# Performance work log

Measured on AMD Instinct MI355X. Metric: run time of the kernel, lower is better.

Reference implementation:

```python
import jax, jax.numpy as jnp
import numpy as np

B, S, D, H = 2, 2048, 512, 8
DK = D // H
DECAY = 0.02
LN_EPS = 1e-5


def setup_inputs() -> dict:
    key = jax.random.key(0)
    ks = jax.random.split(key, 16)
    sd = 1.0 / np.sqrt(D)
    def lin(k, fan_in, fan_out):
        return jax.random.uniform(k, (fan_in, fan_out), jnp.float32, -sd, sd)
    return {
        "x": jax.random.normal(ks[0], (B, S, D), jnp.float32),
        "wq": lin(ks[1], D, D), "bq": jnp.zeros((D,), jnp.float32),
        "wk": lin(ks[2], D, D), "bk": jnp.zeros((D,), jnp.float32),
        "wv": lin(ks[3], D, D), "bv": jnp.zeros((D,), jnp.float32),
        "wo": lin(ks[4], D, D), "bo": jnp.zeros((D,), jnp.float32),
        "g1_w": lin(ks[5], D, D // 2), "g1_b": jnp.zeros((D // 2,), jnp.float32),
        "g2_w": lin(ks[6], D // 2, 1), "g2_b": jnp.zeros((1,), jnp.float32),
        "ln_g": jnp.ones((D,), jnp.float32), "ln_b": jnp.zeros((D,), jnp.float32),
    }


def _temporal_bias(seq_len):
    # exp(-decay * |i-j|) masked to lower triangle (causal), additive bias
    pos = jnp.arange(seq_len)
    dist = jnp.abs(pos[:, None] - pos[None, :]).astype(jnp.float32)
    bias = jnp.exp(-DECAY * dist)
    return jnp.tril(bias)  # (S, S)


def reference(x, wq, bq, wk, bk, wv, bv, wo, bo, g1_w, g1_b, g2_w, g2_b, ln_g, ln_b):
    b, s, d = x.shape
    # projections -> (B, H, S, DK)
    q = (x @ wq + bq).reshape(b, s, H, DK).transpose(0, 2, 1, 3)
    k = (x @ wk + bk).reshape(b, s, H, DK).transpose(0, 2, 1, 3)
    v = (x @ wv + bv).reshape(b, s, H, DK).transpose(0, 2, 1, 3)
    scores = jnp.einsum("bhqd,bhkd->bhqk", q, k) / jnp.sqrt(jnp.float32(DK))
    scores = scores + _temporal_bias(s)[None, None, :, :]
    attn = jax.nn.softmax(scores, axis=-1)  # (B, H, S, S)
    out = jnp.einsum("bhqk,bhkd->bhqd", attn, v)
    out = out.transpose(0, 2, 1, 3).reshape(b, s, d)
    out = out @ wo + bo
    # gated residual
    gate = jax.nn.sigmoid(jax.nn.relu(x @ g1_w + g1_b) @ g2_w + g2_b)  # (B, S, 1)
    out = out * gate + x * (1.0 - gate)
    # layer norm
    mu = jnp.mean(out, axis=-1, keepdims=True)
    var = jnp.var(out, axis=-1, keepdims=True)
    y = (out - mu) / jnp.sqrt(var + LN_EPS) * ln_g + ln_b
    return (y, attn)
```

## Files before the change

kernel.cpp:

```cpp
#include <hip/hip_runtime.h>

#define BB 2
#define SS 2048
#define DD 512
#define HH 8
#define DKK 64
#define NROWS (BB * SS)
#define Y_SIZE (BB * SS * DD)

typedef __attribute__((ext_vector_type(8))) short short8;
typedef __attribute__((ext_vector_type(4))) float f32x4;

__device__ __forceinline__ ushort f2bf(float f) {
  union { float f; unsigned u; } v; v.f = f;
  unsigned u = v.u;
  return (ushort)((u + 0x7fffu + ((u >> 16) & 1u)) >> 16);
}

__device__ __forceinline__ float bf2f(ushort u) {
  union { unsigned u; float f; } v; v.u = ((unsigned)u) << 16;
  return v.f;
}


__global__ __launch_bounds__(256) void conv_x_kernel(const float* __restrict__ x,
                                                     ushort* __restrict__ xb) {
  int i = (blockIdx.x * 256 + threadIdx.x) * 4;
  float4 v = *(const float4*)(x + i);
  ushort4 o = {f2bf(v.x), f2bf(v.y), f2bf(v.z), f2bf(v.w)};
  *(ushort4*)(xb + i) = o;
}

__global__ __launch_bounds__(256) void conv_wt_kernel(
    const float* __restrict__ w0, const float* __restrict__ w1,
    const float* __restrict__ w2, const float* __restrict__ w3,
    ushort* __restrict__ o0, ushort* __restrict__ o1,
    ushort* __restrict__ o2, ushort* __restrict__ o3) {
  __shared__ float T[64][65];
  const float* w; ushort* wt;
  switch (blockIdx.z) {
    case 0: w = w0; wt = o0; break;
    case 1: w = w1; wt = o1; break;
    case 2: w = w2; wt = o2; break;
    default: w = w3; wt = o3; break;
  }
  const int t = threadIdx.x;
  const int n0 = blockIdx.x * 64, k0 = blockIdx.y * 64;
#pragma unroll
  for (int i = 0; i < 4; ++i) {
    int c = t + i * 256;
    int row = c >> 4, cc = c & 15;
    float4 v = *(const float4*)(w + (size_t)(k0 + row) * DD + n0 + cc * 4);
    T[row][cc * 4 + 0] = v.x; T[row][cc * 4 + 1] = v.y;
    T[row][cc * 4 + 2] = v.z; T[row][cc * 4 + 3] = v.w;
  }
  __syncthreads();
#pragma unroll
  for (int i = 0; i < 2; ++i) {
    int c = t + i * 256;
    int nr = c >> 3, kc = c & 7;
    ushort4 a, b;
    a.x = f2bf(T[kc * 8 + 0][nr]); a.y = f2bf(T[kc * 8 + 1][nr]);
    a.z = f2bf(T[kc * 8 + 2][nr]); a.w = f2bf(T[kc * 8 + 3][nr]);
    b.x = f2bf(T[kc * 8 + 4][nr]); b.y = f2bf(T[kc * 8 + 5][nr]);
    b.z = f2bf(T[kc * 8 + 6][nr]); b.w = f2bf(T[kc * 8 + 7][nr]);
    *(ushort4*)(wt + (size_t)(n0 + nr) * DD + k0 + kc * 8) = a;
    *(ushort4*)(wt + (size_t)(n0 + nr) * DD + k0 + kc * 8 + 4) = b;
  }
}


__device__ __forceinline__ void mfma_gemm64(
    const ushort* __restrict__ A, int lda, const ushort* __restrict__ B, int ldb,
    int K, ushort (*As)[72], ushort (*Bs)[72], f32x4 (&acc)[2][2], int t) {
  const int l = t & 63, w = t >> 6;
  const int mq = w & 1, nq = w >> 1;
  const int l15 = l & 15, l4 = l >> 4;
  for (int k0 = 0; k0 < K; k0 += 64) {
    __syncthreads();
#pragma unroll
    for (int i = 0; i < 2; ++i) {
      int c = t + i * 256;
      int row = c >> 3, cc = c & 7;
      *(uint4*)&As[row][cc * 8] = *(const uint4*)(A + (size_t)row * lda + k0 + cc * 8);
      *(uint4*)&Bs[row][cc * 8] = *(const uint4*)(B + (size_t)row * ldb + k0 + cc * 8);
    }
    __syncthreads();
    short8 af[2][2], bf[2][2];
#pragma unroll
    for (int mt = 0; mt < 2; ++mt)
#pragma unroll
      for (int ks = 0; ks < 2; ++ks)
        af[mt][ks] = *(const short8*)&As[32 * mq + 16 * mt + l15][ks * 32 + l4 * 8];
#pragma unroll
    for (int nt = 0; nt < 2; ++nt)
#pragma unroll
      for (int ks = 0; ks < 2; ++ks)
        bf[nt][ks] = *(const short8*)&Bs[32 * nq + 16 * nt + l15][ks * 32 + l4 * 8];
#pragma unroll
    for (int mt = 0; mt < 2; ++mt)
#pragma unroll
      for (int nt = 0; nt < 2; ++nt)
#pragma unroll
        for (int ks = 0; ks < 2; ++ks)
          acc[mt][nt] = __builtin_amdgcn_mfma_f32_16x16x32_bf16(
              af[mt][ks], bf[nt][ks], acc[mt][nt], 0, 0, 0);
  }
}


__global__ __launch_bounds__(256) void proj_qkv_kernel(
    const ushort* __restrict__ xb,
    const ushort* __restrict__ wqt, const float* __restrict__ bq,
    const ushort* __restrict__ wkt, const float* __restrict__ bk,
    const ushort* __restrict__ wvt, const float* __restrict__ bv,
    ushort* __restrict__ qb, ushort* __restrict__ kb, ushort* __restrict__ vt) {
  __shared__ ushort As[64][72], Bs[64][72];
  const ushort* W; const float* bias; ushort* out;
  if (blockIdx.z == 0) { W = wqt; bias = bq; out = qb; }
  else if (blockIdx.z == 1) { W = wkt; bias = bk; out = kb; }
  else { W = wvt; bias = bv; out = vt; }
  const float scale = (blockIdx.z == 0) ? 0.125f : 1.0f;
  const int m0 = blockIdx.x * 64;
  const int h = blockIdx.y;
  const int t = threadIdx.x;
  const int l = t & 63, w = t >> 6;
  const int mq = w & 1, nq = w >> 1;
  const int l15 = l & 15, l4 = l >> 4;
  f32x4 acc[2][2] = {};
  mfma_gemm64(xb + (size_t)m0 * DD, DD, W + (size_t)h * DKK * DD, DD, DD,
              As, Bs, acc, t);
  float biasv[2];
#pragma unroll
  for (int nt = 0; nt < 2; ++nt) biasv[nt] = bias[h * DKK + 32 * nq + 16 * nt + l15];

  if (blockIdx.z < 2) {
    __syncthreads();
#pragma unroll
    for (int mt = 0; mt < 2; ++mt)
#pragma unroll
      for (int nt = 0; nt < 2; ++nt)
#pragma unroll
        for (int r = 0; r < 4; ++r)
          As[32 * mq + 16 * mt + l4 * 4 + r][32 * nq + 16 * nt + l15] =
              f2bf((acc[mt][nt][r] + biasv[nt]) * scale);
    __syncthreads();
#pragma unroll
    for (int i = 0; i < 2; ++i) {
      int c = t + i * 256;
      int row = c >> 3, cc = c & 7;
      int m = m0 + row, b = m >> 11, s = m & (SS - 1);
      uint4 v = *(const uint4*)&As[row][cc * 8];
      *(uint4*)(out + ((size_t)(b * HH + h) * SS + s) * DKK + cc * 8) = v;
    }
  } else {
#pragma unroll
    for (int mt = 0; mt < 2; ++mt)
#pragma unroll
      for (int nt = 0; nt < 2; ++nt) {
        int dk = 32 * nq + 16 * nt + l15;
        int m = m0 + 32 * mq + 16 * mt + l4 * 4;
        int b = m >> 11, sb = m & (SS - 1);
        ushort4 pk;
        pk.x = f2bf(acc[mt][nt][0] + biasv[nt]);
        pk.y = f2bf(acc[mt][nt][1] + biasv[nt]);
        pk.z = f2bf(acc[mt][nt][2] + biasv[nt]);
        pk.w = f2bf(acc[mt][nt][3] + biasv[nt]);
        *(ushort4*)(out + ((size_t)(b * HH + h) * DKK + dk) * SS + sb) = pk;
      }
  }
}


template <int BF16P>
__global__ __launch_bounds__(256) void attn_kernel(
    const ushort* __restrict__ qb, const ushort* __restrict__ kb,
    const ushort* __restrict__ vt, void* __restrict__ pout,
    float* __restrict__ invb, ushort* __restrict__ ctx) {
  __shared__ ushort Ks[64][72], Vs[64][72], Ps[64][72];
  __shared__ float rs[64];
  const int t = threadIdx.x;
  const int l = t & 63, w = t >> 6;
  const int mq = w & 1, nq = w >> 1;
  const int l15 = l & 15, l4 = l >> 4;
  const int z = blockIdx.x;
  const int q0 = blockIdx.y * 64;
  if (t < 64) rs[t] = 0.f;

  short8 qf[2][2];
#pragma unroll
  for (int bt = 0; bt < 2; ++bt)
#pragma unroll
    for (int ks = 0; ks < 2; ++ks)
      qf[bt][ks] = *(const short8*)(qb +
          ((size_t)z * SS + q0 + 32 * mq + 16 * bt + l15) * DKK + ks * 32 + l4 * 8);

  int qi_[2]; float rowf[2];
#pragma unroll
  for (int bt = 0; bt < 2; ++bt) {
    qi_[bt] = q0 + 32 * mq + 16 * bt + l15;
    rowf[bt] = __expf(-0.02f * (float)qi_[bt]);
  }
  const float c_r[4] = {1.0f, 1.0202013f, 1.0408108f, 1.0618365f};

  float rsp[2] = {0.f, 0.f};
  f32x4 oacc[2][2] = {};

  for (int kt = 0; kt < 32; ++kt) {
    __syncthreads();
#pragma unroll
    for (int i = 0; i < 2; ++i) {
      int c = t + i * 256;
      int row = c >> 3, cc = c & 7;
      *(uint4*)&Ks[row][cc * 8] =
          *(const uint4*)(kb + ((size_t)z * SS + kt * 64 + row) * DKK + cc * 8);
      *(uint4*)&Vs[row][cc * 8] =
          *(const uint4*)(vt + ((size_t)z * DKK + row) * SS + kt * 64 + cc * 8);
    }
    __syncthreads();
    short8 kf[2][2];
#pragma unroll
    for (int at = 0; at < 2; ++at)
#pragma unroll
      for (int ks = 0; ks < 2; ++ks)
        kf[at][ks] = *(const short8*)&Ks[32 * nq + 16 * at + l15][ks * 32 + l4 * 8];
    f32x4 acc[2][2] = {};
#pragma unroll
    for (int at = 0; at < 2; ++at)
#pragma unroll
      for (int bt = 0; bt < 2; ++bt)
#pragma unroll
        for (int ks = 0; ks < 2; ++ks)
          acc[at][bt] = __builtin_amdgcn_mfma_f32_16x16x32_bf16(
              kf[at][ks], qf[bt][ks], acc[at][bt], 0, 0, 0);
#pragma unroll
    for (int at = 0; at < 2; ++at) {
      const int kjbase = kt * 64 + 32 * nq + 16 * at + l4 * 4;
      const float colb = __expf(0.02f * (float)kjbase);
#pragma unroll
      for (int bt = 0; bt < 2; ++bt) {
        const float rc = rowf[bt] * colb;
        ushort4 us;
        float pv[4];
#pragma unroll
        for (int r = 0; r < 4; ++r) {
          float bias = (kjbase + r <= qi_[bt]) ? rc * c_r[r] : 0.f;
          float p = __expf(acc[at][bt][r] + bias);
          pv[r] = p;
          rsp[bt] += p;
        }
        us.x = f2bf(pv[0]); us.y = f2bf(pv[1]);
        us.z = f2bf(pv[2]); us.w = f2bf(pv[3]);
        *(ushort4*)&Ps[32 * mq + 16 * bt + l15][32 * nq + 16 * at + l4 * 4] = us;
        const size_t gidx = ((size_t)z * SS + qi_[bt]) * SS + kjbase;
        if (BF16P) {
          *(ushort4*)((ushort*)pout + gidx) = us;
        } else {
          float4 f4 = {pv[0], pv[1], pv[2], pv[3]};
          *(float4*)((float*)pout + gidx) = f4;
        }
      }
    }
    __syncthreads();
    short8 pa[2][2], pb[2][2];
#pragma unroll
    for (int mt = 0; mt < 2; ++mt)
#pragma unroll
      for (int ks = 0; ks < 2; ++ks)
        pa[mt][ks] = *(const short8*)&Ps[32 * mq + 16 * mt + l15][ks * 32 + l4 * 8];
#pragma unroll
    for (int nt = 0; nt < 2; ++nt)
#pragma unroll
      for (int ks = 0; ks < 2; ++ks)
        pb[nt][ks] = *(const short8*)&Vs[32 * nq + 16 * nt + l15][ks * 32 + l4 * 8];
#pragma unroll
    for (int mt = 0; mt < 2; ++mt)
#pragma unroll
      for (int nt = 0; nt < 2; ++nt)
#pragma unroll
        for (int ks = 0; ks < 2; ++ks)
          oacc[mt][nt] = __builtin_amdgcn_mfma_f32_16x16x32_bf16(
              pa[mt][ks], pb[nt][ks], oacc[mt][nt], 0, 0, 0);
  }

#pragma unroll
  for (int bt = 0; bt < 2; ++bt) {
    float v = rsp[bt];
    v += __shfl_xor(v, 16);
    v += __shfl_xor(v, 32);
    if (l < 16) atomicAdd(&rs[32 * mq + 16 * bt + l], v);
  }
  __syncthreads();
  if (t < 64) invb[(size_t)z * SS + q0 + t] = 1.f / rs[t];
  float invr[2][4];
#pragma unroll
  for (int mt = 0; mt < 2; ++mt)
#pragma unroll
    for (int r = 0; r < 4; ++r)
      invr[mt][r] = 1.f / rs[32 * mq + 16 * mt + l4 * 4 + r];

#pragma unroll
  for (int mt = 0; mt < 2; ++mt)
#pragma unroll
    for (int nt = 0; nt < 2; ++nt)
#pragma unroll
      for (int r = 0; r < 4; ++r)
        Ps[32 * mq + 16 * mt + l4 * 4 + r][32 * nq + 16 * nt + l15] =
            f2bf(oacc[mt][nt][r] * invr[mt][r]);
  __syncthreads();
  const int b = z >> 3, h = z & 7;
#pragma unroll
  for (int i = 0; i < 2; ++i) {
    int c = t + i * 256;
    int row = c >> 3, cc = c & 7;
    uint4 v = *(const uint4*)&Ps[row][cc * 8];
    *(uint4*)(ctx + ((size_t)(b * SS + q0 + row)) * DD + h * DKK + cc * 8) = v;
  }
}


__global__ __launch_bounds__(256) void scale_attn_bf(
    const ushort* __restrict__ pbuf, const float* __restrict__ invb,
    float* __restrict__ attn) {
  const size_t row = blockIdx.x;
  const float inv = invb[row];
  const int t = threadIdx.x;
  const size_t base = row * SS + t * 8;
  uint4 u = *(const uint4*)(pbuf + base);
  const ushort* us = (const ushort*)&u;
  float4 a, b;
  a.x = bf2f(us[0]) * inv; a.y = bf2f(us[1]) * inv;
  a.z = bf2f(us[2]) * inv; a.w = bf2f(us[3]) * inv;
  b.x = bf2f(us[4]) * inv; b.y = bf2f(us[5]) * inv;
  b.z = bf2f(us[6]) * inv; b.w = bf2f(us[7]) * inv;
  *(float4*)(attn + base) = a;
  *(float4*)(attn + base + 4) = b;
}

__global__ __launch_bounds__(256) void scale_attn_f32(
    float* __restrict__ attn, const float* __restrict__ invb) {
  const size_t row = blockIdx.x;
  const float inv = invb[row];
  const int t = threadIdx.x;
  const size_t base = row * SS + t * 8;
  float4 a = *(const float4*)(attn + base);
  float4 b = *(const float4*)(attn + base + 4);
  a.x *= inv; a.y *= inv; a.z *= inv; a.w *= inv;
  b.x *= inv; b.y *= inv; b.z *= inv; b.w *= inv;
  *(float4*)(attn + base) = a;
  *(float4*)(attn + base + 4) = b;
}


__global__ __launch_bounds__(256) void proj_o_kernel(
    const ushort* __restrict__ ctx, const ushort* __restrict__ wot,
    const float* __restrict__ bo, float* __restrict__ o) {
  __shared__ ushort As[64][72], Bs[64][72];
  const int m0 = blockIdx.x * 64, n0 = blockIdx.y * 64;
  const int t = threadIdx.x;
  const int l = t & 63, w = t >> 6;
  const int mq = w & 1, nq = w >> 1;
  const int l15 = l & 15, l4 = l >> 4;
  f32x4 acc[2][2] = {};
  mfma_gemm64(ctx + (size_t)m0 * DD, DD, wot + (size_t)n0 * DD, DD, DD,
              As, Bs, acc, t);
#pragma unroll
  for (int nt = 0; nt < 2; ++nt) {
    int col = n0 + 32 * nq + 16 * nt + l15;
    float bv = bo[col];
#pragma unroll
    for (int mt = 0; mt < 2; ++mt)
#pragma unroll
      for (int r = 0; r < 4; ++r) {
        int m = m0 + 32 * mq + 16 * mt + l4 * 4 + r;
        o[(size_t)m * DD + col] = acc[mt][nt][r] + bv;
      }
  }
}


__global__ __launch_bounds__(256) void gate_kernel(
    const float* __restrict__ x, const float* __restrict__ g1w,
    const float* __restrict__ g1b, const float* __restrict__ g2w,
    const float* __restrict__ g2b, float* __restrict__ gate) {
  __shared__ float xs[8][512];
  __shared__ float red[32];
  const int r0 = blockIdx.x * 8;
  const int t = threadIdx.x;
  const float4* xg = (const float4*)&x[(size_t)r0 * DD];
  float4* xsv = (float4*)&xs[0][0];
#pragma unroll
  for (int i = 0; i < 4; ++i) xsv[t + i * 256] = xg[t + i * 256];
  __syncthreads();
  float acc[8] = {};
  for (int i = 0; i < 512; i += 4) {
    float w0 = g1w[(i + 0) * 256 + t];
    float w1 = g1w[(i + 1) * 256 + t];
    float w2 = g1w[(i + 2) * 256 + t];
    float w3 = g1w[(i + 3) * 256 + t];
#pragma unroll
    for (int r = 0; r < 8; ++r) {
      float4 xv = *(const float4*)&xs[r][i];
      acc[r] += xv.x * w0 + xv.y * w1 + xv.z * w2 + xv.w * w3;
    }
  }
  float b1 = g1b[t], w2_ = g2w[t];
  float p[8];
#pragma unroll
  for (int r = 0; r < 8; ++r) {
    float h = acc[r] + b1;
    h = h > 0.f ? h : 0.f;
    p[r] = h * w2_;
  }
#pragma unroll
  for (int r = 0; r < 8; ++r)
    for (int off = 32; off; off >>= 1) p[r] += __shfl_xor(p[r], off, 64);
  if ((t & 63) == 0) {
#pragma unroll
    for (int r = 0; r < 8; ++r) red[r * 4 + (t >> 6)] = p[r];
  }
  __syncthreads();
  if (t < 8) {
    float s = red[t * 4] + red[t * 4 + 1] + red[t * 4 + 2] + red[t * 4 + 3] + g2b[0];
    gate[r0 + t] = 1.f / (1.f + __expf(-s));
  }
}


__global__ __launch_bounds__(256) void blend_ln_kernel(
    const float* __restrict__ o, const float* __restrict__ x,
    const float* __restrict__ gate, const float* __restrict__ ln_g,
    const float* __restrict__ ln_b, float* __restrict__ y) {
  __shared__ float r1[4], r2[4];
  const int row = blockIdx.x, t = threadIdx.x;
  float g = gate[row];
  float2 o2 = *(const float2*)&o[(size_t)row * DD + t * 2];
  float2 x2 = *(const float2*)&x[(size_t)row * DD + t * 2];
  float va = o2.x * g + x2.x * (1.f - g);
  float vb = o2.y * g + x2.y * (1.f - g);
  float s = va + vb, q = va * va + vb * vb;
  for (int off = 32; off; off >>= 1) {
    s += __shfl_xor(s, off, 64);
    q += __shfl_xor(q, off, 64);
  }
  if ((t & 63) == 0) { r1[t >> 6] = s; r2[t >> 6] = q; }
  __syncthreads();
  s = r1[0] + r1[1] + r1[2] + r1[3];
  q = r2[0] + r2[1] + r2[2] + r2[3];
  float mean = s * (1.f / 512.f);
  float var = q * (1.f / 512.f) - mean * mean;
  float rstd = rsqrtf(var + 1e-5f);
  float2 lg = *(const float2*)&ln_g[t * 2];
  float2 lb = *(const float2*)&ln_b[t * 2];
  float2 out;
  out.x = (va - mean) * rstd * lg.x + lb.x;
  out.y = (vb - mean) * rstd * lg.y + lb.y;
  *(float2*)&y[(size_t)row * DD + t * 2] = out;
}

extern "C" void kernel_launch(void* const* d_in, const int* in_sizes, int n_in,
                              void* d_out, int out_size, void* d_ws, size_t ws_size,
                              hipStream_t stream) {
  const float* x   = (const float*)d_in[0];
  const float* wq  = (const float*)d_in[1];
  const float* bq  = (const float*)d_in[2];
  const float* wk  = (const float*)d_in[3];
  const float* bk  = (const float*)d_in[4];
  const float* wv  = (const float*)d_in[5];
  const float* bv  = (const float*)d_in[6];
  const float* wo  = (const float*)d_in[7];
  const float* bo  = (const float*)d_in[8];
  const float* g1w = (const float*)d_in[9];
  const float* g1b = (const float*)d_in[10];
  const float* g2w = (const float*)d_in[11];
  const float* g2b = (const float*)d_in[12];
  const float* lng = (const float*)d_in[13];
  const float* lnb = (const float*)d_in[14];

  float* y    = (float*)d_out;
  float* attn = y + (size_t)Y_SIZE;

  char* ws = (char*)d_ws;
  ushort* xb  = (ushort*)(ws);
  ushort* wqt = (ushort*)(ws + (4 << 20));
  ushort* wkt = (ushort*)(ws + (4 << 20) + (512 << 10));
  ushort* wvt = (ushort*)(ws + (5 << 20));
  ushort* wot = (ushort*)(ws + (5 << 20) + (512 << 10));
  ushort* qb  = (ushort*)(ws + (6 << 20));
  ushort* kb  = (ushort*)(ws + (10 << 20));
  ushort* vt  = (ushort*)(ws + (14 << 20));
  ushort* ctx = (ushort*)(ws + (18 << 20));
  float*  o   = (float*)(ws + (22 << 20));
  float*  gate= (float*)(ws + (30 << 20));
  float*  invb= (float*)(ws + (30 << 20) + (256 << 10));
  ushort* pbuf= (ushort*)(ws + (32 << 20));

  const bool bigws = ws_size >= ((size_t)168 << 20);

  hipLaunchKernelGGL(conv_x_kernel, dim3(Y_SIZE / 1024), dim3(256), 0, stream, x, xb);
  hipLaunchKernelGGL(conv_wt_kernel, dim3(8, 8, 4), dim3(256), 0, stream,
                     wq, wk, wv, wo, wqt, wkt, wvt, wot);
  hipLaunchKernelGGL(proj_qkv_kernel, dim3(64, 8, 3), dim3(256), 0, stream,
                     xb, wqt, bq, wkt, bk, wvt, bv, qb, kb, vt);
  hipLaunchKernelGGL(gate_kernel, dim3(512), dim3(256), 0, stream,
                     x, g1w, g1b, g2w, g2b, gate);
  if (bigws) {
    hipLaunchKernelGGL(attn_kernel<1>, dim3(16, 32), dim3(256), 0, stream,
                       qb, kb, vt, (void*)pbuf, invb, ctx);
    hipLaunchKernelGGL(scale_attn_bf, dim3(BB * HH * SS), dim3(256), 0, stream,
                       pbuf, invb, attn);
  } else {
    hipLaunchKernelGGL(attn_kernel<0>, dim3(16, 32), dim3(256), 0, stream,
                       qb, kb, vt, (void*)attn, invb, ctx);
    hipLaunchKernelGGL(scale_attn_f32, dim3(BB * HH * SS), dim3(256), 0, stream,
                       attn, invb);
  }
  hipLaunchKernelGGL(proj_o_kernel, dim3(64, 8), dim3(256), 0, stream,
                     ctx, wot, bo, o);
  hipLaunchKernelGGL(blend_ln_kernel, dim3(4096), dim3(256), 0, stream,
                     o, x, gate, lng, lnb, y);
}
```

Before: 484.7 us.

## Recompute QK^T in a second pass to write normalized attn directly

The attention kernel no longer writes unnormalized probabilities to a scratch buffer for a separate scaling kernel to rescale. After computing the row sums and context, it runs a second pass over all K tiles with double-buffered shared memory, recomputes scores and exp, and writes the normalized fp32 attention matrix straight to the output. This removes the intermediate round trip and the extra scale kernel in exchange for doubling the QK^T MFMA and exp work. The grid is also transposed so that consecutive blocks share the same head.

```diff
diff --git a/kernel.cpp b/kernel.cpp
--- a/kernel.cpp
+++ b/kernel.cpp
@@ -15,11 +15,6 @@
   union { float f; unsigned u; } v; v.f = f;
   unsigned u = v.u;
   return (ushort)((u + 0x7fffu + ((u >> 16) & 1u)) >> 16);
-}
-
-__device__ __forceinline__ float bf2f(ushort u) {
-  union { unsigned u; float f; } v; v.u = ((unsigned)u) << 16;
-  return v.f;
 }
 
 
@@ -172,19 +167,18 @@
 }
 
 
-template <int BF16P>
 __global__ __launch_bounds__(256) void attn_kernel(
     const ushort* __restrict__ qb, const ushort* __restrict__ kb,
-    const ushort* __restrict__ vt, void* __restrict__ pout,
-    float* __restrict__ invb, ushort* __restrict__ ctx) {
+    const ushort* __restrict__ vt, float* __restrict__ attn,
+    ushort* __restrict__ ctx) {
   __shared__ ushort Ks[64][72], Vs[64][72], Ps[64][72];
   __shared__ float rs[64];
   const int t = threadIdx.x;
   const int l = t & 63, w = t >> 6;
   const int mq = w & 1, nq = w >> 1;
   const int l15 = l & 15, l4 = l >> 4;
-  const int z = blockIdx.x;
-  const int q0 = blockIdx.y * 64;
+  const int z = blockIdx.y;
+  const int q0 = blockIdx.x * 64;
   if (t < 64) rs[t] = 0.f;
 
   short8 qf[2][2];
@@ -252,13 +246,6 @@
         us.x = f2bf(pv[0]); us.y = f2bf(pv[1]);
         us.z = f2bf(pv[2]); us.w = f2bf(pv[3]);
         *(ushort4*)&Ps[32 * mq + 16 * bt + l15][32 * nq + 16 * at + l4 * 4] = us;
-        const size_t gidx = ((size_t)z * SS + qi_[bt]) * SS + kjbase;
-        if (BF16P) {
-          *(ushort4*)((ushort*)pout + gidx) = us;
-        } else {
-          float4 f4 = {pv[0], pv[1], pv[2], pv[3]};
-          *(float4*)((float*)pout + gidx) = f4;
-        }
       }
     }
     __syncthreads();
@@ -291,7 +278,9 @@
     if (l < 16) atomicAdd(&rs[32 * mq + 16 * bt + l], v);
   }
   __syncthreads();
-  if (t < 64) invb[(size_t)z * SS + q0 + t] = 1.f / rs[t];
+  float invq[2];
+#pragma unroll
+  for (int bt = 0; bt < 2; ++bt) invq[bt] = 1.f / rs[32 * mq + 16 * bt + l15];
   float invr[2][4];
 #pragma unroll
   for (int mt = 0; mt < 2; ++mt)
@@ -308,47 +297,73 @@
         Ps[32 * mq + 16 * mt + l4 * 4 + r][32 * nq + 16 * nt + l15] =
             f2bf(oacc[mt][nt][r] * invr[mt][r]);
   __syncthreads();
-  const int b = z >> 3, h = z & 7;
-#pragma unroll
-  for (int i = 0; i < 2; ++i) {
-    int c = t + i * 256;
-    int row = c >> 3, cc = c & 7;
-    uint4 v = *(const uint4*)&Ps[row][cc * 8];
-    *(uint4*)(ctx + ((size_t)(b * SS + q0 + row)) * DD + h * DKK + cc * 8) = v;
-  }
-}
-
-
-__global__ __launch_bounds__(256) void scale_attn_bf(
-    const ushort* __restrict__ pbuf, const float* __restrict__ invb,
-    float* __restrict__ attn) {
-  const size_t row = blockIdx.x;
-  const float inv = invb[row];
-  const int t = threadIdx.x;
-  const size_t base = row * SS + t * 8;
-  uint4 u = *(const uint4*)(pbuf + base);
-  const ushort* us = (const ushort*)&u;
-  float4 a, b;
-  a.x = bf2f(us[0]) * inv; a.y = bf2f(us[1]) * inv;
-  a.z = bf2f(us[2]) * inv; a.w = bf2f(us[3]) * inv;
-  b.x = bf2f(us[4]) * inv; b.y = bf2f(us[5]) * inv;
-  b.z = bf2f(us[6]) * inv; b.w = bf2f(us[7]) * inv;
-  *(float4*)(attn + base) = a;
-  *(float4*)(attn + base + 4) = b;
-}
-
-__global__ __launch_bounds__(256) void scale_attn_f32(
-    float* __restrict__ attn, const float* __restrict__ invb) {
-  const size_t row = blockIdx.x;
-  const float inv = invb[row];
-  const int t = threadIdx.x;
-  const size_t base = row * SS + t * 8;
-  float4 a = *(const float4*)(attn + base);
-  float4 b = *(const float4*)(attn + base + 4);
-  a.x *= inv; a.y *= inv; a.z *= inv; a.w *= inv;
-  b.x *= inv; b.y *= inv; b.z *= inv; b.w *= inv;
-  *(float4*)(attn + base) = a;
-  *(float4*)(attn + base + 4) = b;
+  {
+    const int b = z >> 3, h = z & 7;
+#pragma unroll
+    for (int i = 0; i < 2; ++i) {
+      int c = t + i * 256;
+      int row = c >> 3, cc = c & 7;
+      uint4 v = *(const uint4*)&Ps[row][cc * 8];
+      *(uint4*)(ctx + ((size_t)(b * SS + q0 + row)) * DD + h * DKK + cc * 8) = v;
+    }
+  }
+
+  const int srow = t >> 3, scol = (t & 7) * 8;
+  const int srow2 = srow + 32;
+  __syncthreads();
+  {
+    const ushort* p = kb + (size_t)z * SS * DKK;
+    *(uint4*)&Ks[srow][scol]  = *(const uint4*)(p + (size_t)srow * DKK + scol);
+    *(uint4*)&Ks[srow2][scol] = *(const uint4*)(p + (size_t)srow2 * DKK + scol);
+  }
+  __syncthreads();
+  for (int kt = 0; kt < 32; ++kt) {
+    ushort (*cur)[72] = (kt & 1) ? Vs : Ks;
+    ushort (*nxt)[72] = (kt & 1) ? Ks : Vs;
+    uint4 s0, s1;
+    if (kt < 31) {
+      const ushort* p = kb + ((size_t)z * SS + (kt + 1) * 64) * DKK;
+      s0 = *(const uint4*)(p + (size_t)srow * DKK + scol);
+      s1 = *(const uint4*)(p + (size_t)srow2 * DKK + scol);
+    }
+    short8 kf[2][2];
+#pragma unroll
+    for (int at = 0; at < 2; ++at)
+#pragma unroll
+      for (int ks = 0; ks < 2; ++ks)
+        kf[at][ks] = *(const short8*)&cur[32 * nq + 16 * at + l15][ks * 32 + l4 * 8];
+    f32x4 acc[2][2] = {};
+#pragma unroll
+    for (int at = 0; at < 2; ++at)
+#pragma unroll
+      for (int bt = 0; bt < 2; ++bt)
+#pragma unroll
+        for (int ks = 0; ks < 2; ++ks)
+          acc[at][bt] = __builtin_amdgcn_mfma_f32_16x16x32_bf16(
+              kf[at][ks], qf[bt][ks], acc[at][bt], 0, 0, 0);
+#pragma unroll
+    for (int at = 0; at < 2; ++at) {
+      const int kjbase = kt * 64 + 32 * nq + 16 * at + l4 * 4;
+      const float colb = __expf(0.02f * (float)kjbase);
+#pragma unroll
+      for (int bt = 0; bt < 2; ++bt) {
+        const float rc = rowf[bt] * colb;
+        float4 f4;
+#pragma unroll
+        for (int r = 0; r < 4; ++r) {
+          float bias = (kjbase + r <= qi_[bt]) ? rc * c_r[r] : 0.f;
+          float p = __expf(acc[at][bt][r] + bias) * invq[bt];
+          ((float*)&f4)[r] = p;
+        }
+        *(float4*)(attn + ((size_t)z * SS + qi_[bt]) * SS + kjbase) = f4;
+      }
+    }
+    if (kt < 31) {
+      *(uint4*)&nxt[srow][scol]  = s0;
+      *(uint4*)&nxt[srow2][scol] = s1;
+    }
+    __syncthreads();
+  }
 }
 
 
@@ -492,10 +507,6 @@
   ushort* ctx = (ushort*)(ws + (18 << 20));
   float*  o   = (float*)(ws + (22 << 20));
   float*  gate= (float*)(ws + (30 << 20));
-  float*  invb= (float*)(ws + (30 << 20) + (256 << 10));
-  ushort* pbuf= (ushort*)(ws + (32 << 20));
-
-  const bool bigws = ws_size >= ((size_t)168 << 20);
 
   hipLaunchKernelGGL(conv_x_kernel, dim3(Y_SIZE / 1024), dim3(256), 0, stream, x, xb);
   hipLaunchKernelGGL(conv_wt_kernel, dim3(8, 8, 4), dim3(256), 0, stream,
@@ -504,17 +515,8 @@
                      xb, wqt, bq, wkt, bk, wvt, bv, qb, kb, vt);
   hipLaunchKernelGGL(gate_kernel, dim3(512), dim3(256), 0, stream,
                      x, g1w, g1b, g2w, g2b, gate);
-  if (bigws) {
-    hipLaunchKernelGGL(attn_kernel<1>, dim3(16, 32), dim3(256), 0, stream,
-                       qb, kb, vt, (void*)pbuf, invb, ctx);
-    hipLaunchKernelGGL(scale_attn_bf, dim3(BB * HH * SS), dim3(256), 0, stream,
-                       pbuf, invb, attn);
-  } else {
-    hipLaunchKernelGGL(attn_kernel<0>, dim3(16, 32), dim3(256), 0, stream,
-                       qb, kb, vt, (void*)attn, invb, ctx);
-    hipLaunchKernelGGL(scale_attn_f32, dim3(BB * HH * SS), dim3(256), 0, stream,
-                       attn, invb);
-  }
+  hipLaunchKernelGGL(attn_kernel, dim3(32, 16), dim3(256), 0, stream,
+                     qb, kb, vt, attn, ctx);
   hipLaunchKernelGGL(proj_o_kernel, dim3(64, 8), dim3(256), 0, stream,
                      ctx, wot, bo, o);
   hipLaunchKernelGGL(blend_ln_kernel, dim3(4096), dim3(256), 0, stream,
```

After: 458.9 us. -5.3%, faster.
